# Kernel tuning notes

Hardware: AMD Instinct MI355X
Metric: run time of the kernel (lower is better)

The kernel has to match this reference:

```python
import jax, jax.numpy as jnp
import numpy as np

Q = 4          # base of nested scalar quantizer (config.q)
M = 2          # hierarchy depth (config.M)
LEVELS = Q ** M  # total number of representable integer levels
SCALE = 60.0   # manual scale_factor passed to the layer
EPS = 1e-8


def _scalar_quantize(x):
    # Symmetric nested-lattice scalar quantizer over q^M integer levels:
    # round to nearest integer, clip to the symmetric range covered by the
    # M-level base-q codebook.
    half = LEVELS // 2
    return jnp.clip(jnp.round(x), -half, half - 1)


def _ste_quantize_weight(w):
    # Per-row L2 norm scaling -> unit-norm rows -> scale by SCALE -> quantize
    # -> rescale back (matches ScalarStraightThroughQuantize.forward).
    row_norms = jnp.linalg.norm(w, axis=1, keepdims=True)          # [out, 1]
    row_norms_safe = jnp.maximum(row_norms, EPS)
    w_scaled = w / row_norms_safe * SCALE
    q = _scalar_quantize(w_scaled)
    return q * row_norms_safe / SCALE


def setup_inputs() -> dict:
    key = jax.random.key(0)
    k1, k2 = jax.random.split(key)
    BATCH, IN_F, OUT_F = 8192, 4096, 4096
    x = jax.random.normal(k1, (BATCH, IN_F), dtype=jnp.float32)
    # weight initialized as randn * 0.1 per the module
    weight = jax.random.normal(k2, (OUT_F, IN_F), dtype=jnp.float32) * 0.1
    bias = jnp.zeros((OUT_F,), dtype=jnp.float32)
    return {"x": x, "weight": weight, "bias": bias}


def reference(x, weight, bias):
    # STE: forward uses the quantized weight; gradient is identity through
    # the quantizer (stop_gradient trick).
    w_q = weight + jax.lax.stop_gradient(_ste_quantize_weight(weight) - weight)
    return x @ w_q.T + bias
```

## Files before the change

### kernel.cpp

```cpp
#include <hip/hip_runtime.h>
#include <hip/hip_bf16.h>


typedef int int32x4 __attribute__((ext_vector_type(4)));

#define MDIM 8192
#define NDIM 4096
#define KDIM 4096

__device__ __forceinline__ void async_copy16(const void* g, void* l) {
  __builtin_amdgcn_global_load_lds(
      (const __attribute__((address_space(1))) void*)g,
      (__attribute__((address_space(3))) void*)l, 16, 0, 0);
}

__device__ __forceinline__ unsigned pack4(float a, float b, float c, float d) {
  return ((unsigned)((int)a & 0xff)) | ((unsigned)((int)b & 0xff) << 8) |
         ((unsigned)((int)c & 0xff) << 16) | ((unsigned)((int)d & 0xff) << 24);
}

__global__ __launch_bounds__(256) void quantize_all(
    const float* __restrict__ w, const float* __restrict__ x,
    unsigned* __restrict__ qw, unsigned* __restrict__ qx,
    float* __restrict__ scale, float* __restrict__ sx) {
  const int t = threadIdx.x;
  __shared__ float wred[4];
  if (blockIdx.x < NDIM) {
    const int row = blockIdx.x;
    const float4* wr = (const float4*)(w + (size_t)row * KDIM);
    float4 v[4];
    float ss = 0.f;
#pragma unroll
    for (int i = 0; i < 4; ++i) {
      v[i] = wr[t + 256 * i];
      ss += v[i].x * v[i].x + v[i].y * v[i].y + v[i].z * v[i].z + v[i].w * v[i].w;
    }
#pragma unroll
    for (int m = 32; m >= 1; m >>= 1) ss += __shfl_xor(ss, m, 64);
    if ((t & 63) == 0) wred[t >> 6] = ss;
    __syncthreads();
    const float safe = fmaxf(sqrtf(wred[0] + wred[1] + wred[2] + wred[3]), 1e-8f);
    unsigned* qr = qw + (size_t)row * (KDIM / 4);
#pragma unroll
    for (int i = 0; i < 4; ++i) {
      float q0 = fminf(fmaxf(rintf(v[i].x / safe * 60.0f), -8.f), 7.f);
      float q1 = fminf(fmaxf(rintf(v[i].y / safe * 60.0f), -8.f), 7.f);
      float q2 = fminf(fmaxf(rintf(v[i].z / safe * 60.0f), -8.f), 7.f);
      float q3 = fminf(fmaxf(rintf(v[i].w / safe * 60.0f), -8.f), 7.f);
      qr[t + 256 * i] = pack4(q0, q1, q2, q3);
    }
    if (t == 0) scale[row] = safe / 60.0f;
  } else {
    const int row = blockIdx.x - NDIM;
    const float4* xr = (const float4*)(x + (size_t)row * KDIM);
    float4 v[4];
    float am = 0.f;
#pragma unroll
    for (int i = 0; i < 4; ++i) {
      v[i] = xr[t + 256 * i];
      am = fmaxf(am, fmaxf(fmaxf(fabsf(v[i].x), fabsf(v[i].y)),
                           fmaxf(fabsf(v[i].z), fabsf(v[i].w))));
    }
#pragma unroll
    for (int m = 32; m >= 1; m >>= 1) am = fmaxf(am, __shfl_xor(am, m, 64));
    if ((t & 63) == 0) wred[t >> 6] = am;
    __syncthreads();
    const float amax =
        fmaxf(fmaxf(fmaxf(wred[0], wred[1]), fmaxf(wred[2], wred[3])), 1e-20f);
    const float r = 127.0f / amax;
    unsigned* qr = qx + (size_t)row * (KDIM / 4);
#pragma unroll
    for (int i = 0; i < 4; ++i) {
      float q0 = fminf(fmaxf(rintf(v[i].x * r), -127.f), 127.f);
      float q1 = fminf(fmaxf(rintf(v[i].y * r), -127.f), 127.f);
      float q2 = fminf(fmaxf(rintf(v[i].z * r), -127.f), 127.f);
      float q3 = fminf(fmaxf(rintf(v[i].w * r), -127.f), 127.f);
      qr[t + 256 * i] = pack4(q0, q1, q2, q3);
    }
    if (t == 0) sx[row] = amax / 127.0f;
  }
}

__global__ __launch_bounds__(256, 2) void gemm_i8(const char* __restrict__ A,
                                                  const char* __restrict__ B,
                                                  const float* __restrict__ sx,
                                                  const float* __restrict__ scale,
                                                  const float* __restrict__ bias,
                                                  float* __restrict__ C) {
  __shared__ __align__(16) char sA[128 * 128];
  __shared__ __align__(16) char sB[256 * 128];
  const int tid = threadIdx.x;
  const int m0 = blockIdx.y * 128;
  const int n0 = blockIdx.x * 256;

  const int r0 = tid >> 3;
  const int c16 = ((tid & 7) ^ ((tid >> 3) & 7)) * 16;
  const char* gA = A + (size_t)(m0 + r0) * KDIM + c16;
  const char* gB = B + (size_t)(n0 + r0) * KDIM + c16;
  char* lA = sA + tid * 16;
  char* lB = sB + tid * 16;

  const int lane = tid & 63;
  const int wid = tid >> 6;
  const int wm = (wid & 1) * 64;
  const int wn = (wid >> 1) * 128;
  const int fr = lane & 15;
  const int q = lane >> 4;
  const int sw = fr & 7;
  const int ph0 = ((q) ^ sw) * 16;
  const int ph1 = ((4 + q) ^ sw) * 16;

  int32x4 acc[4][8] = {};

  for (int kt = 0; kt < KDIM / 128; ++kt) {
    __syncthreads();
#pragma unroll
    for (int i = 0; i < 4; ++i)
      async_copy16(gA + (size_t)(32 * i) * KDIM, lA + i * 4096);
#pragma unroll
    for (int i = 0; i < 8; ++i)
      async_copy16(gB + (size_t)(32 * i) * KDIM, lB + i * 4096);
    __syncthreads();
    gA += 128; gB += 128;

#pragma unroll
    for (int h = 0; h < 2; ++h) {
      const int ph = h ? ph1 : ph0;
      int32x4 af[4], bg[8];
#pragma unroll
      for (int i = 0; i < 4; ++i)
        af[i] = *(const int32x4*)&sA[(wm + i * 16 + fr) * 128 + ph];
#pragma unroll
      for (int j = 0; j < 8; ++j)
        bg[j] = *(const int32x4*)&sB[(wn + j * 16 + fr) * 128 + ph];
#pragma unroll
      for (int i = 0; i < 4; ++i)
#pragma unroll
        for (int j = 0; j < 8; ++j)
          acc[i][j] =
              __builtin_amdgcn_mfma_i32_16x16x64_i8(af[i], bg[j], acc[i][j], 0, 0, 0);
    }
  }

  float scl[8], bs[8];
#pragma unroll
  for (int j = 0; j < 8; ++j) {
    const int n = n0 + wn + j * 16 + fr;
    scl[j] = scale[n];
    bs[j] = bias[n];
  }
  const int mrow = q * 4;
#pragma unroll
  for (int i = 0; i < 4; ++i) {
#pragma unroll
    for (int r = 0; r < 4; ++r) {
      const size_t m = (size_t)(m0 + wm + i * 16 + mrow + r);
      const float sxm = sx[m];
      float* crow = C + m * NDIM + (n0 + wn + fr);
#pragma unroll
      for (int j = 0; j < 8; ++j)
        crow[j * 16] = (float)acc[i][j][r] * (sxm * scl[j]) + bs[j];
    }
  }
}

extern "C" void kernel_launch(void* const* d_in, const int* in_sizes, int n_in,
                              void* d_out, int out_size, void* d_ws, size_t ws_size,
                              hipStream_t stream) {
  (void)in_sizes; (void)n_in; (void)out_size; (void)ws_size;
  const float* x = (const float*)d_in[0];
  const float* w = (const float*)d_in[1];
  const float* bias = (const float*)d_in[2];
  float* out = (float*)d_out;

  char* ws = (char*)d_ws;
  char* qx = ws;
  char* qw = ws + (size_t)33554432;
  float* sx = (float*)(ws + (size_t)50331648);
  float* scale = (float*)(ws + (size_t)50331648 + 65536);

  quantize_all<<<NDIM + MDIM, 256, 0, stream>>>(w, x, (unsigned*)qw,
                                                (unsigned*)qx, scale, sx);
  dim3 grid(NDIM / 256, MDIM / 128);
  gemm_i8<<<grid, 256, 0, stream>>>(qx, qw, sx, scale, bias, out);
}
```

Baseline: 377.2 us.

## Rewrite int8 GEMM as 256x256 tile, 8-wave, double-buffered ping-pong pipeline

Replaces the single-buffered 128x256 int8 GEMM with a 256x256 block tile run by 512 threads (8 waves). The K loop is split into 64-byte half-steps held in a two-deep LDS buffer, so async global-to-LDS copies for upcoming K slices overlap the MFMA work on the current one. Barrier, wait-count and setprio phases alternate the waves between loading and computing. It also adds a grid swizzle for L2 locality and a new LDS XOR swizzle. In exchange it uses 128KB of LDS per block and depends on hand-counted vmcnt waits, which are fragile if the copy count or order changes.

```diff
diff --git a/kernel.cpp b/kernel.cpp
--- a/kernel.cpp
+++ b/kernel.cpp
@@ -81,85 +81,136 @@
   }
 }
 
-__global__ __launch_bounds__(256, 2) void gemm_i8(const char* __restrict__ A,
+
+#define STAGE(dst, gbase, kt, kh)                                   \
+  do {                                                              \
+    const char* _g = (gbase) + (kt) * 128 + (kh) * 64;              \
+    async_copy16(_g, (dst) + t16);                                  \
+    async_copy16(_g + (size_t)128 * KDIM, (dst) + 8192 + t16);      \
+  } while (0)
+
+#define LDB(d, h)                                                   \
+  _Pragma("unroll") for (int j = 0; j < 4; ++j) bg[j] =             \
+      *(const int32x4*)(&sB[d][h][0] + boff + j * 1024);
+
+#define LDA(d, h, mb)                                               \
+  _Pragma("unroll") for (int ia = 0; ia < 4; ++ia) af[ia] =         \
+      *(const int32x4*)(&sA[d][h][0] + aoff + ((mb) + ia) * 1024);
+
+#define MFMA_BLK(mb)                                                \
+  _Pragma("unroll") for (int ic = 0; ic < 4; ++ic)                  \
+  _Pragma("unroll") for (int j = 0; j < 4; ++j)                     \
+      acc[(mb) + ic][j] = __builtin_amdgcn_mfma_i32_16x16x64_i8(    \
+          af[ic], bg[j], acc[(mb) + ic][j], 0, 0, 0);
+
+#define PH_SYNC1()                                                  \
+  __builtin_amdgcn_s_barrier();                                     \
+  asm volatile("s_waitcnt lgkmcnt(0)" ::: "memory");                \
+  __builtin_amdgcn_sched_barrier(0);                                \
+  __builtin_amdgcn_s_setprio(1);
+
+#define PH_SYNC2()                                                  \
+  __builtin_amdgcn_s_setprio(0);                                    \
+  __builtin_amdgcn_sched_barrier(0);                                \
+  __builtin_amdgcn_s_barrier();
+
+#define PH_SYNC2V()                                                 \
+  __builtin_amdgcn_s_setprio(0);                                    \
+  __builtin_amdgcn_sched_barrier(0);                                \
+  asm volatile("s_waitcnt vmcnt(6)" ::: "memory");                  \
+  __builtin_amdgcn_s_barrier();
+
+__global__ __launch_bounds__(512, 2) void gemm_i8(const char* __restrict__ A,
                                                   const char* __restrict__ B,
                                                   const float* __restrict__ sx,
                                                   const float* __restrict__ scale,
                                                   const float* __restrict__ bias,
                                                   float* __restrict__ C) {
-  __shared__ __align__(16) char sA[128 * 128];
-  __shared__ __align__(16) char sB[256 * 128];
-  const int tid = threadIdx.x;
-  const int m0 = blockIdx.y * 128;
-  const int n0 = blockIdx.x * 256;
-
-  const int r0 = tid >> 3;
-  const int c16 = ((tid & 7) ^ ((tid >> 3) & 7)) * 16;
-  const char* gA = A + (size_t)(m0 + r0) * KDIM + c16;
-  const char* gB = B + (size_t)(n0 + r0) * KDIM + c16;
-  char* lA = sA + tid * 16;
-  char* lB = sB + tid * 16;
-
-  const int lane = tid & 63;
-  const int wid = tid >> 6;
-  const int wm = (wid & 1) * 64;
-  const int wn = (wid >> 1) * 128;
+  __shared__ __align__(16) char sA[2][2][16384];
+  __shared__ __align__(16) char sB[2][2][16384];
+  const int t = threadIdx.x;
+  const int t16 = t * 16;
+
+  const int bid = blockIdx.x;
+  const int swz = (bid & 7) * 64 + (bid >> 3);
+  const int m0 = (swz >> 4) * 256;
+  const int n0 = (swz & 15) * 256;
+
+  const int srow = t >> 2;
+  const int c4s = (t & 3) ^ ((srow >> 1) & 3);
+  const char* gA0 = A + (size_t)(m0 + srow) * KDIM + c4s * 16;
+  const char* gB0 = B + (size_t)(n0 + srow) * KDIM + c4s * 16;
+
+  const int lane = t & 63;
+  const int wid = t >> 6;
+  const int wm = (wid & 1) * 128;
+  const int wn = (wid >> 1) * 64;
   const int fr = lane & 15;
   const int q = lane >> 4;
-  const int sw = fr & 7;
-  const int ph0 = ((q) ^ sw) * 16;
-  const int ph1 = ((4 + q) ^ sw) * 16;
-
-  int32x4 acc[4][8] = {};
-
-  for (int kt = 0; kt < KDIM / 128; ++kt) {
-    __syncthreads();
-#pragma unroll
-    for (int i = 0; i < 4; ++i)
-      async_copy16(gA + (size_t)(32 * i) * KDIM, lA + i * 4096);
-#pragma unroll
-    for (int i = 0; i < 8; ++i)
-      async_copy16(gB + (size_t)(32 * i) * KDIM, lB + i * 4096);
-    __syncthreads();
-    gA += 128; gB += 128;
-
-#pragma unroll
-    for (int h = 0; h < 2; ++h) {
-      const int ph = h ? ph1 : ph0;
-      int32x4 af[4], bg[8];
-#pragma unroll
-      for (int i = 0; i < 4; ++i)
-        af[i] = *(const int32x4*)&sA[(wm + i * 16 + fr) * 128 + ph];
-#pragma unroll
-      for (int j = 0; j < 8; ++j)
-        bg[j] = *(const int32x4*)&sB[(wn + j * 16 + fr) * 128 + ph];
-#pragma unroll
-      for (int i = 0; i < 4; ++i)
-#pragma unroll
-        for (int j = 0; j < 8; ++j)
-          acc[i][j] =
-              __builtin_amdgcn_mfma_i32_16x16x64_i8(af[i], bg[j], acc[i][j], 0, 0, 0);
-    }
-  }
-
-  float scl[8], bs[8];
-#pragma unroll
-  for (int j = 0; j < 8; ++j) {
+  const int qs = (q ^ ((fr >> 1) & 3)) * 16;
+  const int aoff = (wm + fr) * 64 + qs;
+  const int boff = (wn + fr) * 64 + qs;
+
+  int32x4 acc[8][4] = {};
+  int32x4 af[4], bg[4];
+
+  STAGE(&sA[0][0][0], gA0, 0, 0);
+  STAGE(&sA[0][1][0], gA0, 0, 1);
+  STAGE(&sB[0][0][0], gB0, 0, 0);
+  STAGE(&sB[0][1][0], gB0, 0, 1);
+  STAGE(&sB[1][0][0], gB0, 1, 0);
+  STAGE(&sA[1][0][0], gA0, 1, 0);
+  STAGE(&sB[1][1][0], gB0, 1, 1);
+  asm volatile("s_waitcnt vmcnt(6)" ::: "memory");
+  __builtin_amdgcn_s_barrier();
+
+  for (int it = 0; it < 16; ++it) {
+    const int kt2 = (2 * it + 2) & 31;
+    const int kt3 = (2 * it + 3) & 31;
+    LDB(0, 0); LDA(0, 0, 0);
+    STAGE(&sA[1][1][0], gA0, 2 * it + 1, 1);
+    PH_SYNC1(); MFMA_BLK(0); PH_SYNC2();
+    LDA(0, 0, 4);
+    STAGE(&sB[0][0][0], gB0, kt2, 0);
+    PH_SYNC1(); MFMA_BLK(4); PH_SYNC2();
+    LDB(0, 1); LDA(0, 1, 0);
+    STAGE(&sA[0][0][0], gA0, kt2, 0);
+    PH_SYNC1(); MFMA_BLK(0); PH_SYNC2();
+    LDA(0, 1, 4);
+    STAGE(&sB[0][1][0], gB0, kt2, 1);
+    PH_SYNC1(); MFMA_BLK(4); PH_SYNC2V();
+    LDB(1, 0); LDA(1, 0, 0);
+    STAGE(&sA[0][1][0], gA0, kt2, 1);
+    PH_SYNC1(); MFMA_BLK(0); PH_SYNC2();
+    LDA(1, 0, 4);
+    STAGE(&sB[1][0][0], gB0, kt3, 0);
+    PH_SYNC1(); MFMA_BLK(4); PH_SYNC2();
+    LDB(1, 1); LDA(1, 1, 0);
+    STAGE(&sA[1][0][0], gA0, kt3, 0);
+    PH_SYNC1(); MFMA_BLK(0); PH_SYNC2();
+    LDA(1, 1, 4);
+    STAGE(&sB[1][1][0], gB0, kt3, 1);
+    PH_SYNC1(); MFMA_BLK(4); PH_SYNC2V();
+  }
+
+  float scl[4], bs[4];
+#pragma unroll
+  for (int j = 0; j < 4; ++j) {
     const int n = n0 + wn + j * 16 + fr;
     scl[j] = scale[n];
     bs[j] = bias[n];
   }
   const int mrow = q * 4;
 #pragma unroll
-  for (int i = 0; i < 4; ++i) {
+  for (int im = 0; im < 8; ++im) {
 #pragma unroll
     for (int r = 0; r < 4; ++r) {
-      const size_t m = (size_t)(m0 + wm + i * 16 + mrow + r);
+      const size_t m = (size_t)(m0 + wm + im * 16 + mrow + r);
       const float sxm = sx[m];
       float* crow = C + m * NDIM + (n0 + wn + fr);
 #pragma unroll
-      for (int j = 0; j < 8; ++j)
-        crow[j * 16] = (float)acc[i][j][r] * (sxm * scl[j]) + bs[j];
+      for (int j = 0; j < 4; ++j)
+        crow[j * 16] = (float)acc[im][j][r] * (sxm * scl[j]) + bs[j];
     }
   }
 }
@@ -181,6 +232,5 @@
 
   quantize_all<<<NDIM + MDIM, 256, 0, stream>>>(w, x, (unsigned*)qw,
                                                 (unsigned*)qx, scale, sx);
-  dim3 grid(NDIM / 256, MDIM / 128);
-  gemm_i8<<<grid, 256, 0, stream>>>(qx, qw, sx, scale, bias, out);
-}
+  gemm_i8<<<512, 512, 0, stream>>>(qx, qw, sx, scale, bias, out);
+}
```

Result: slower. 385.9 us (+2.3%).

## Double-buffer int8 GEMM LDS tiles with K=64 stages and raise MFMA priority

Applied to the files above, without the earlier changes.

Replaces the single-buffered 128-wide K tile, which used a sync-load-sync pattern, with two 64-wide K buffers. The async global-to-LDS copy for the next tile is issued before computing the current one, so load latency can overlap with MFMA work. The LDS swizzle is reworked for 64-byte rows, and s_setprio raises wave priority around the MFMA block. The last iteration issues a redundant wrapped load of tile 0, and halving K per stage doubles the number of barriers.

```diff
diff --git a/kernel.cpp b/kernel.cpp
--- a/kernel.cpp
+++ b/kernel.cpp
@@ -81,24 +81,50 @@
   }
 }
 
+
+#define STAGE_TILE(nb, kt)                                                 \
+  do {                                                                     \
+    const char* _ga = gA0 + (kt) * 64;                                     \
+    const char* _gb = gB0 + (kt) * 64;                                     \
+    async_copy16(_ga, &sA[nb][tid * 16]);                                  \
+    async_copy16(_ga + (size_t)64 * KDIM, &sA[nb][4096 + tid * 16]);       \
+    async_copy16(_gb, &sB[nb][tid * 16]);                                  \
+    async_copy16(_gb + (size_t)64 * KDIM, &sB[nb][4096 + tid * 16]);       \
+    async_copy16(_gb + (size_t)128 * KDIM, &sB[nb][8192 + tid * 16]);      \
+    async_copy16(_gb + (size_t)192 * KDIM, &sB[nb][12288 + tid * 16]);     \
+  } while (0)
+
+#define COMPUTE(cb)                                                        \
+  do {                                                                     \
+    int32x4 af[4], bg[8];                                                  \
+    _Pragma("unroll") for (int i = 0; i < 4; ++i)                          \
+        af[i] = *(const int32x4*)&sA[cb][(wm + i * 16 + fr) * 64 + qs];    \
+    _Pragma("unroll") for (int j = 0; j < 8; ++j)                          \
+        bg[j] = *(const int32x4*)&sB[cb][(wn + j * 16 + fr) * 64 + qs];    \
+    __builtin_amdgcn_s_setprio(1);                                         \
+    _Pragma("unroll") for (int i = 0; i < 4; ++i)                          \
+    _Pragma("unroll") for (int j = 0; j < 8; ++j)                          \
+        acc[i][j] = __builtin_amdgcn_mfma_i32_16x16x64_i8(af[i], bg[j],    \
+                                                          acc[i][j], 0, 0, 0); \
+    __builtin_amdgcn_s_setprio(0);                                         \
+  } while (0)
+
 __global__ __launch_bounds__(256, 2) void gemm_i8(const char* __restrict__ A,
                                                   const char* __restrict__ B,
                                                   const float* __restrict__ sx,
                                                   const float* __restrict__ scale,
                                                   const float* __restrict__ bias,
                                                   float* __restrict__ C) {
-  __shared__ __align__(16) char sA[128 * 128];
-  __shared__ __align__(16) char sB[256 * 128];
+  __shared__ __align__(16) char sA[2][8192];
+  __shared__ __align__(16) char sB[2][16384];
   const int tid = threadIdx.x;
   const int m0 = blockIdx.y * 128;
   const int n0 = blockIdx.x * 256;
 
-  const int r0 = tid >> 3;
-  const int c16 = ((tid & 7) ^ ((tid >> 3) & 7)) * 16;
-  const char* gA = A + (size_t)(m0 + r0) * KDIM + c16;
-  const char* gB = B + (size_t)(n0 + r0) * KDIM + c16;
-  char* lA = sA + tid * 16;
-  char* lB = sB + tid * 16;
+  const int srow = tid >> 2;
+  const int c4s = (tid & 3) ^ ((srow >> 1) & 3);
+  const char* gA0 = A + (size_t)(m0 + srow) * KDIM + c4s * 16;
+  const char* gB0 = B + (size_t)(n0 + srow) * KDIM + c4s * 16;
 
   const int lane = tid & 63;
   const int wid = tid >> 6;
@@ -106,40 +132,20 @@
   const int wn = (wid >> 1) * 128;
   const int fr = lane & 15;
   const int q = lane >> 4;
-  const int sw = fr & 7;
-  const int ph0 = ((q) ^ sw) * 16;
-  const int ph1 = ((4 + q) ^ sw) * 16;
+  const int qs = (q ^ ((fr >> 1) & 3)) * 16;
 
   int32x4 acc[4][8] = {};
 
-  for (int kt = 0; kt < KDIM / 128; ++kt) {
+  STAGE_TILE(0, 0);
+  __syncthreads();
+
+  for (int it = 0; it < 32; ++it) {
+    STAGE_TILE(1, 2 * it + 1);
+    COMPUTE(0);
     __syncthreads();
-#pragma unroll
-    for (int i = 0; i < 4; ++i)
-      async_copy16(gA + (size_t)(32 * i) * KDIM, lA + i * 4096);
-#pragma unroll
-    for (int i = 0; i < 8; ++i)
-      async_copy16(gB + (size_t)(32 * i) * KDIM, lB + i * 4096);
+    STAGE_TILE(0, (2 * it + 2) & 63);
+    COMPUTE(1);
     __syncthreads();
-    gA += 128; gB += 128;
-
-#pragma unroll
-    for (int h = 0; h < 2; ++h) {
-      const int ph = h ? ph1 : ph0;
-      int32x4 af[4], bg[8];
-#pragma unroll
-      for (int i = 0; i < 4; ++i)
-        af[i] = *(const int32x4*)&sA[(wm + i * 16 + fr) * 128 + ph];
-#pragma unroll
-      for (int j = 0; j < 8; ++j)
-        bg[j] = *(const int32x4*)&sB[(wn + j * 16 + fr) * 128 + ph];
-#pragma unroll
-      for (int i = 0; i < 4; ++i)
-#pragma unroll
-        for (int j = 0; j < 8; ++j)
-          acc[i][j] =
-              __builtin_amdgcn_mfma_i32_16x16x64_i8(af[i], bg[j], acc[i][j], 0, 0, 0);
-    }
   }
 
   float scl[8], bs[8];
```

Measured after the change: 403.2 us. 6.9% more time.
